# Kernel optimization log

Measured on AMD Instinct MI355X. Metric: run time of the kernel, lower is better.

## Reference

```python
import jax, jax.numpy as jnp
import numpy as np

N, E = 50000, 500000
A, R, EB, EH, H, C, AH, SH, S, AV = 64, 20, 32, 64, 4, 32, 128, 64, 32, 32
EPS = 1e-8
MAX_DIST = 0.5   # nm, maximum_interaction_radius
SCALE = 1.0      # nm, scale_factor


def physnet_rbf(d):
    # PhysNet radial basis: exp(-beta * (exp(-d) - mu_k)^2), mu_k in [exp(-r_cut), 1]
    mu = jnp.linspace(np.exp(-MAX_DIST), 1.0, R).astype(jnp.float32)
    beta = jnp.float32((2.0 / R * (1.0 - np.exp(-MAX_DIST))) ** -2)
    return jnp.exp(-beta * (jnp.exp(-d)[:, None] - mu) ** 2)  # [E, R]


def _forward(h, x, v, idx_i, idx_j, W_edge_in, b_edge_in, W_edge_h, b_edge_h,
             W_edge_out, b_edge_out, W_att, b_att, W_x_mix, W_node1, b_node1,
             W_node2, b_node2, W_post1, b_post1, W_post2, b_post2,
             W_vel1, b_vel1, W_vel2, w_v_mix):
    n = h.shape[0]
    act = jax.nn.silu
    seg_sum = lambda t, idx: jax.ops.segment_sum(t, idx, num_segments=n)

    # geometry
    r_ij = x[idx_j] - x[idx_i]                       # [E,3]
    d_ij = jnp.sqrt(jnp.sum(r_ij * r_ij, -1) + EPS)  # [E]
    dir_ij = r_ij / (d_ij[:, None] + EPS)            # [E,3]

    # update_edge: gather, RBF filter, edge MLP
    h_cat = jnp.concatenate([h[idx_i], h[idx_j]], -1)                 # [E,2A]
    filtered = physnet_rbf(d_ij) * (h_cat @ W_edge_in + b_edge_in)    # [E,R]
    e_in = jnp.concatenate([h_cat, filtered, d_ij[:, None] / SCALE], -1)
    h_ij_edge = act(e_in @ W_edge_h + b_edge_h) @ W_edge_out + b_edge_out  # [E,EB]

    # semantic attention: CELU logits + segment softmax over receivers per head
    logits = jax.nn.celu(h_ij_edge @ W_att + b_att, alpha=2.0)        # [E,H]
    seg_max = jax.ops.segment_max(logits, idx_i, num_segments=n)      # [n,H]
    exp_l = jnp.exp(logits - seg_max[idx_i])
    denom = seg_sum(exp_l, idx_i)
    att = exp_l / (denom[idx_i] + EPS)                                # [E,H]
    h_ij_semantic = (att[:, :, None] * h_ij_edge[:, None, :]).reshape(-1, H * EB)

    # neighborhood aggregation (scatter-add)
    h_i_semantic = seg_sum(h_ij_semantic, idx_i)                      # [n,H*EB]

    # spatial attention
    mix = jnp.tanh(h_ij_semantic @ W_x_mix)                           # [E,C]
    combinations = dir_ij[:, None, :] * mix[:, :, None]               # [E,C,3]
    counts = jnp.maximum(seg_sum(jnp.ones((idx_i.shape[0],), h.dtype), idx_i), 1.0)
    comb_mean = seg_sum(combinations, idx_i) / counts[:, None, None]  # scatter-mean
    comb_norm2 = jnp.sum(comb_mean * comb_mean, -1)                   # [n,C]
    h_i_spatial = act(act(comb_norm2 @ W_post1 + b_post1) @ W_post2 + b_post2)

    # node update (residual)
    node_in = jnp.concatenate([h, h_i_semantic, h_i_spatial], -1)
    h_upd = h + act(act(node_in @ W_node1 + b_node1) @ W_node2 + b_node2)

    # velocity / coordinate update
    v_ij = jnp.einsum('ecx,c->ex', combinations, w_v_mix)             # [E,3]
    dv = seg_sum(v_ij, idx_i) / counts[:, None]                       # scatter-mean
    gate = 2.0 * jax.nn.sigmoid(act(h_upd @ W_vel1 + b_vel1) @ W_vel2)  # [n,1]
    v_upd = gate * v + dv
    x_upd = x + v_upd
    return h_upd, x_upd, v_upd


def _p(k, shape, scale=0.05):
    return jax.random.normal(k, shape, dtype=jnp.float32) * scale


def setup_inputs() -> dict:
    key = jax.random.key(0)
    ks = jax.random.split(key, 24)
    return {
        'h': jax.random.normal(ks[0], (N, A), dtype=jnp.float32),
        'x': jax.random.normal(ks[1], (N, 3), dtype=jnp.float32),
        'v': jax.random.normal(ks[2], (N, 3), dtype=jnp.float32),
        'idx_i': jax.random.randint(ks[3], (E,), 0, N),
        'idx_j': jax.random.randint(ks[4], (E,), 0, N),
        'W_edge_in': _p(ks[5], (2 * A, R)), 'b_edge_in': jnp.zeros((R,), jnp.float32),
        'W_edge_h': _p(ks[6], (2 * A + R + 1, EH)), 'b_edge_h': jnp.zeros((EH,), jnp.float32),
        'W_edge_out': _p(ks[7], (EH, EB)), 'b_edge_out': jnp.zeros((EB,), jnp.float32),
        'W_att': _p(ks[8], (EB, H)), 'b_att': jnp.zeros((H,), jnp.float32),
        'W_x_mix': _p(ks[9], (H * EB, C)),
        'W_node1': _p(ks[10], (A + H * EB + S, AH)), 'b_node1': jnp.zeros((AH,), jnp.float32),
        'W_node2': _p(ks[11], (AH, A)), 'b_node2': jnp.zeros((A,), jnp.float32),
        'W_post1': _p(ks[12], (C, SH)), 'b_post1': jnp.zeros((SH,), jnp.float32),
        'W_post2': _p(ks[13], (SH, S)), 'b_post2': jnp.zeros((S,), jnp.float32),
        'W_vel1': _p(ks[14], (A, AV)), 'b_vel1': jnp.zeros((AV,), jnp.float32),
        'W_vel2': _p(ks[15], (AV, 1)),
        'w_v_mix': _p(ks[16], (C,)),
    }


def reference(h, x, v, idx_i, idx_j, W_edge_in, b_edge_in, W_edge_h, b_edge_h,
              W_edge_out, b_edge_out, W_att, b_att, W_x_mix, W_node1, b_node1,
              W_node2, b_node2, W_post1, b_post1, W_post2, b_post2,
              W_vel1, b_vel1, W_vel2, w_v_mix):
    return _forward(h, x, v, idx_i, idx_j, W_edge_in, b_edge_in, W_edge_h, b_edge_h,
                    W_edge_out, b_edge_out, W_att, b_att, W_x_mix, W_node1, b_node1,
                    W_node2, b_node2, W_post1, b_post1, W_post2, b_post2,
                    W_vel1, b_vel1, W_vel2, w_v_mix)
```

## Files before the change

kernel.cpp:

```cpp
#include <hip/hip_runtime.h>
#include <math.h>

#define DA 64
#define NODEIN_DIM 224
#define EPSC 1e-8f

typedef short v8s __attribute__((ext_vector_type(8)));
typedef float v4f __attribute__((ext_vector_type(4)));
typedef unsigned short ushort_t;

__device__ __forceinline__ float siluf(float v) { return v / (1.0f + __expf(-v)); }

__device__ __forceinline__ void atomAddF(float* p, float v) {
#if defined(__HIP_DEVICE_COMPILE__)
  unsafeAtomicAdd(p, v);
#else
  atomicAdd(p, v);
#endif
}

__device__ __forceinline__ unsigned short f2bfu(float f) {
  union { float f; unsigned u; } v; v.f = f;
  unsigned r = v.u + 0x7fffu + ((v.u >> 16) & 1u);
  return (unsigned short)(r >> 16);
}
__device__ __forceinline__ short f2bfs(float f) { return (short)f2bfu(f); }
__device__ __forceinline__ float bf2f(ushort_t s) {
  union { unsigned u; float f; } v; v.u = ((unsigned)s) << 16; return v.f;
}

#define MU0 0.60653065971263342f
#define DMU ((1.0f - 0.60653065971263342f) / 19.0f)
#define BETA ((float)(1.0 / (0.039346934028736658 * 0.039346934028736658)))

__global__ __launch_bounds__(256) void cast_h(
    const float* __restrict__ hsrc, ushort_t* __restrict__ hb, int n4)
{
  const int i = blockIdx.x * blockDim.x + threadIdx.x;
  if (i < n4) {
    const float4 fv = ((const float4*)hsrc)[i];
    ushort4 o;
    o.x = f2bfu(fv.x); o.y = f2bfu(fv.y); o.z = f2bfu(fv.z); o.w = f2bfu(fv.w);
    ((ushort4*)hb)[i] = o;
  }
}

__global__ __launch_bounds__(256) void deg_count(
    const int* __restrict__ idx_i, int* __restrict__ deg, int E)
{
  const int stride = gridDim.x * blockDim.x;
  for (int e = blockIdx.x * blockDim.x + threadIdx.x; e < E; e += stride)
    atomicAdd(&deg[idx_i[e]], 1);
}

#define SCAN_B 64
#define SCAN_T (SCAN_B * 256)

__global__ __launch_bounds__(256) void deg_tsum(
    const int* __restrict__ deg, int* __restrict__ tsum, int N, int C)
{
  const int g = blockIdx.x * blockDim.x + threadIdx.x;
  const int lo = g * C;
  const int hi = (lo + C < N) ? (lo + C) : N;
  int s = 0;
  for (int i = lo; i < hi; ++i) s += deg[i];
  tsum[g] = s;
}

__global__ __launch_bounds__(256) void scan_tsum(int* __restrict__ tsum)
{
  __shared__ int ps[256];
  const int t = threadIdx.x;
  const int per = SCAN_T / 256;
  const int lo = t * per;
  int s = 0;
  for (int i = 0; i < per; ++i) s += tsum[lo + i];
  ps[t] = s;
  __syncthreads();
  if (t == 0) {
    int a = 0;
    for (int i = 0; i < 256; ++i) { const int v = ps[i]; ps[i] = a; a += v; }
  }
  __syncthreads();
  int acc = ps[t];
  for (int i = 0; i < per; ++i) {
    const int v = tsum[lo + i];
    tsum[lo + i] = acc;
    acc += v;
  }
}

__global__ __launch_bounds__(256) void write_csr(
    const int* __restrict__ deg, const int* __restrict__ tpre,
    int* __restrict__ rowstart, int* __restrict__ cursor,
    float* __restrict__ counts, int N, int C)
{
  const int g = blockIdx.x * blockDim.x + threadIdx.x;
  const int lo = g * C;
  const int hi = (lo + C < N) ? (lo + C) : N;
  int acc = tpre[g];
  for (int i = lo; i < hi; ++i) {
    const int d = deg[i];
    rowstart[i] = acc;
    cursor[i] = acc;
    counts[i] = (float)d;
    acc += d;
  }
  if (hi == N) rowstart[N] = acc;
}

__global__ __launch_bounds__(256) void bucket_edges(
    const int* __restrict__ idx_i, const int* __restrict__ idx_j,
    int* __restrict__ cursor, int* __restrict__ iperm,
    int* __restrict__ jperm, int E)
{
  const int stride = gridDim.x * blockDim.x;
  for (int e = blockIdx.x * blockDim.x + threadIdx.x; e < E; e += stride) {
    const int ii = idx_i[e];
    const int pos = atomicAdd(&cursor[ii], 1);
    iperm[pos] = ii;
    jperm[pos] = idx_j[e];
  }
}

#define THS 72
__global__ __launch_bounds__(256) void edge_f12(
    const ushort_t* __restrict__ h_bf, const float* __restrict__ x,
    const int* __restrict__ iperm, const int* __restrict__ jperm,
    const float* __restrict__ W_in, const float* __restrict__ b_in,
    const float* __restrict__ W_h, const float* __restrict__ b_h,
    const float* __restrict__ W_out, const float* __restrict__ b_out,
    const float* __restrict__ W_att, const float* __restrict__ b_att,
    float* __restrict__ dirb, ushort_t* __restrict__ heb,
    float* __restrict__ expl, float* __restrict__ denom, int E)
{
  __shared__ ushort_t sB1[8 * 512];
  __shared__ ushort_t sB2[20 * 512];
  __shared__ ushort_t tH[4][16 * THS];

  const int tid = threadIdx.x;
  for (int idx = tid; idx < 8 * 512; idx += 256) {
    const int j = idx & 7;
    const int ln = (idx >> 3) & 63;
    const int f = idx >> 9;
    const int k = (f >> 1) * 32 + (ln >> 4) * 8 + j;
    const int col = (f & 1) * 16 + (ln & 15);
    sB1[idx] = (col < 20) ? f2bfu(W_in[k * 20 + col]) : (ushort_t)0;
  }
  for (int idx = tid; idx < 20 * 512; idx += 256) {
    const int j = idx & 7;
    const int ln = (idx >> 3) & 63;
    const int f = idx >> 9;
    const int k = (f >> 2) * 32 + (ln >> 4) * 8 + j;
    const int col = (f & 3) * 16 + (ln & 15);
    sB2[idx] = (k < 149) ? f2bfu(W_h[k * 64 + col]) : (ushort_t)0;
  }
  __syncthreads();

  const int gtid = blockIdx.x * blockDim.x + tid;
  const int wid = gtid >> 6;
  const int lane = tid & 63;
  const int w = tid >> 6;
  const int nw = (gridDim.x * blockDim.x) >> 6;
  const int l15 = lane & 15;
  const int q = lane >> 4;

  const ushort_t* b1l = sB1 + lane * 8;
  const ushort_t* b2l = sB2 + lane * 8;

  v8s bfr3[2][2];
  #pragma unroll
  for (int kc = 0; kc < 2; ++kc)
    #pragma unroll
    for (int nt = 0; nt < 2; ++nt)
      #pragma unroll
      for (int j = 0; j < 8; ++j) {
        const int k = kc * 32 + q * 8 + j;
        const int col = nt * 16 + l15;
        bfr3[kc][nt][j] = f2bfs(W_out[k * 32 + col]);
      }

  float bin[2], mu[2];
  #pragma unroll
  for (int nt = 0; nt < 2; ++nt) {
    const int col = nt * 16 + l15;
    bin[nt] = (col < 20) ? b_in[col] : 0.0f;
    mu[nt] = MU0 + (float)col * DMU;
  }
  float bias2[4];
  #pragma unroll
  for (int nt = 0; nt < 4; ++nt) bias2[nt] = b_h[nt * 16 + l15];
  float bias3[2];
  #pragma unroll
  for (int nt = 0; nt < 2; ++nt) bias3[nt] = b_out[nt * 16 + l15];

  v8s battf;
  #pragma unroll
  for (int j = 0; j < 8; ++j)
    battf[j] = (l15 < 4) ? f2bfs(W_att[(q * 8 + j) * 4 + l15]) : (short)0;
  const float bav = (l15 < 4) ? b_att[l15] : 0.0f;

  const int ntiles = (E + 15) >> 4;

  int iiC = 0, jjC = 0;
  v8s afr[4];
  if (wid < ntiles) {
    const int row0 = wid * 16 + l15;
    const int rowL0 = (row0 < E) ? row0 : (E - 1);
    iiC = iperm[rowL0];
    jjC = jperm[rowL0];
    afr[0] = *(const v8s*)(h_bf + (size_t)iiC * 64 + q * 8);
    afr[1] = *(const v8s*)(h_bf + (size_t)iiC * 64 + 32 + q * 8);
    afr[2] = *(const v8s*)(h_bf + (size_t)jjC * 64 + q * 8);
    afr[3] = *(const v8s*)(h_bf + (size_t)jjC * 64 + 32 + q * 8);
  }

  for (int t = wid; t < ntiles; t += nw) {
    const int tn = t + nw;
    int iiN = 0, jjN = 0;
    v8s nfr[4];
    if (tn < ntiles) {
      const int rowN = tn * 16 + l15;
      const int rowLN = (rowN < E) ? rowN : (E - 1);
      iiN = iperm[rowLN];
      jjN = jperm[rowLN];
      nfr[0] = *(const v8s*)(h_bf + (size_t)iiN * 64 + q * 8);
      nfr[1] = *(const v8s*)(h_bf + (size_t)iiN * 64 + 32 + q * 8);
      nfr[2] = *(const v8s*)(h_bf + (size_t)jjN * 64 + q * 8);
      nfr[3] = *(const v8s*)(h_bf + (size_t)jjN * 64 + 32 + q * 8);
    }

    const int row = t * 16 + l15;
    float dval = 0.0f;
    if (lane < 16 && row < E) {
      const float rx = x[jjC * 3 + 0] - x[iiC * 3 + 0];
      const float ry = x[jjC * 3 + 1] - x[iiC * 3 + 1];
      const float rz = x[jjC * 3 + 2] - x[iiC * 3 + 2];
      const float d = sqrtf(rx * rx + ry * ry + rz * rz + EPSC);
      dval = d;
      const float inv = 1.0f / (d + EPSC);
      dirb[row * 3 + 0] = rx * inv;
      dirb[row * 3 + 1] = ry * inv;
      dirb[row * 3 + 2] = rz * inv;
    }

    v4f acc1[2];
    #pragma unroll
    for (int nt = 0; nt < 2; ++nt) {
      v4f a = {0.f, 0.f, 0.f, 0.f};
      #pragma unroll
      for (int kc = 0; kc < 4; ++kc) {
        const v8s bfrag = *(const v8s*)(b1l + (kc * 2 + nt) * 512);
        a = __builtin_amdgcn_mfma_f32_16x16x32_bf16(afr[kc], bfrag, a, 0, 0, 0);
      }
      acc1[nt] = a;
    }

    float dr[4], edr[4];
    #pragma unroll
    for (int r = 0; r < 4; ++r) {
      dr[r] = __shfl(dval, q * 4 + r);
      edr[r] = __expf(-dr[r]);
    }
    #pragma unroll
    for (int nt = 0; nt < 2; ++nt) {
      const int col = nt * 16 + l15;
      #pragma unroll
      for (int r = 0; r < 4; ++r) {
        ushort_t ov;
        if (col < 20) {
          const float tt = edr[r] - mu[nt];
          ov = f2bfu((acc1[nt][r] + bin[nt]) * __expf(-BETA * tt * tt));
        } else if (col == 20) {
          ov = f2bfu(dr[r]);
        } else {
          ov = 0;
        }
        tH[w][(q * 4 + r) * THS + col] = ov;
      }
    }
    __builtin_amdgcn_wave_barrier();

    const v8s afr4 = *(const v8s*)&tH[w][l15 * THS + q * 8];
    __builtin_amdgcn_wave_barrier();

    v4f acc2[4];
    #pragma unroll
    for (int nt = 0; nt < 4; ++nt) {
      v4f a = {0.f, 0.f, 0.f, 0.f};
      #pragma unroll
      for (int kc = 0; kc < 4; ++kc) {
        const v8s bfrag = *(const v8s*)(b2l + (kc * 4 + nt) * 512);
        a = __builtin_amdgcn_mfma_f32_16x16x32_bf16(afr[kc], bfrag, a, 0, 0, 0);
      }
      const v8s bfrag4 = *(const v8s*)(b2l + (4 * 4 + nt) * 512);
      a = __builtin_amdgcn_mfma_f32_16x16x32_bf16(afr4, bfrag4, a, 0, 0, 0);
      acc2[nt] = a;
    }

    #pragma unroll
    for (int nt = 0; nt < 4; ++nt) {
      #pragma unroll
      for (int r = 0; r < 4; ++r)
        tH[w][(q * 4 + r) * THS + nt * 16 + l15] =
            f2bfu(siluf(acc2[nt][r] + bias2[nt]));
    }
    __builtin_amdgcn_wave_barrier();

    v8s af3[2];
    af3[0] = *(const v8s*)&tH[w][l15 * THS + q * 8];
    af3[1] = *(const v8s*)&tH[w][l15 * THS + 32 + q * 8];

    v4f acc3[2];
    #pragma unroll
    for (int nt = 0; nt < 2; ++nt) {
      v4f a = {0.f, 0.f, 0.f, 0.f};
      #pragma unroll
      for (int kc = 0; kc < 2; ++kc)
        a = __builtin_amdgcn_mfma_f32_16x16x32_bf16(af3[kc], bfr3[kc][nt], a, 0, 0, 0);
      acc3[nt] = a;
    }
    __builtin_amdgcn_wave_barrier();

    const int rowb = t * 16 + q * 4;
    #pragma unroll
    for (int nt = 0; nt < 2; ++nt) {
      const int col = nt * 16 + l15;
      #pragma unroll
      for (int r = 0; r < 4; ++r) {
        const ushort_t hv = f2bfu(acc3[nt][r] + bias3[nt]);
        tH[w][(q * 4 + r) * THS + col] = hv;
        if (rowb + r < E) heb[(size_t)(rowb + r) * 32 + col] = hv;
      }
    }
    __builtin_amdgcn_wave_barrier();

    const v8s afA = *(const v8s*)&tH[w][l15 * THS + q * 8];
    v4f az = {0.f, 0.f, 0.f, 0.f};
    const v4f aacc = __builtin_amdgcn_mfma_f32_16x16x32_bf16(afA, battf, az, 0, 0, 0);

    int ii_r[4];
    #pragma unroll
    for (int r = 0; r < 4; ++r) ii_r[r] = __shfl(iiC, q * 4 + r);

    if (l15 < 4) {
      #pragma unroll
      for (int r = 0; r < 4; ++r) {
        if (rowb + r < E) {
          const float la = aacc[r] + bav;
          const float l = (la > 0.f) ? la : 2.0f * (__expf(0.5f * la) - 1.0f);
          const float ev = __expf(l);
          expl[(size_t)(rowb + r) * 4 + l15] = ev;
          atomAddF(&denom[ii_r[r] * 4 + l15], ev);
        }
      }
    }
    __builtin_amdgcn_wave_barrier();

    iiC = iiN; jjC = jjN;
    afr[0] = nfr[0]; afr[1] = nfr[1]; afr[2] = nfr[2]; afr[3] = nfr[3];
  }
}

__global__ __launch_bounds__(256) void mix_kernel(
    const ushort_t* __restrict__ heb, const int* __restrict__ iperm,
    const float* __restrict__ expl, const float* __restrict__ denom,
    const float* __restrict__ W_xmix, const float* __restrict__ w_vmix,
    ushort_t* __restrict__ mixE, float* __restrict__ pE, int E)
{
  const int tid = blockIdx.x * blockDim.x + threadIdx.x;
  const int wid = tid >> 6;
  const int lane = threadIdx.x & 63;
  const int nw = (gridDim.x * blockDim.x) >> 6;
  const int l15 = lane & 15;
  const int q = lane >> 4;

  v8s bfr[4][2];
  #pragma unroll
  for (int kc = 0; kc < 4; ++kc)
    #pragma unroll
    for (int nt = 0; nt < 2; ++nt)
      #pragma unroll
      for (int j = 0; j < 8; ++j) {
        const int k = kc * 32 + q * 8 + j;
        const int col = nt * 16 + l15;
        bfr[kc][nt][j] = f2bfs(W_xmix[k * 32 + col]);
      }
  float wv[2];
  wv[0] = w_vmix[l15];
  wv[1] = w_vmix[16 + l15];

  const int ntiles = (E + 15) >> 4;
  for (int t = wid; t < ntiles; t += nw) {
    const int row = t * 16 + l15;
    const int rowL = (row < E) ? row : (E - 1);
    const int ii = iperm[rowL];
    float att[4];
    #pragma unroll
    for (int hh = 0; hh < 4; ++hh)
      att[hh] = expl[(size_t)rowL * 4 + hh] / (denom[ii * 4 + hh] + EPSC);

    const v8s hech = *(const v8s*)(heb + (size_t)rowL * 32 + q * 8);
    float hef[8];
    #pragma unroll
    for (int j = 0; j < 8; ++j) hef[j] = bf2f((ushort_t)hech[j]);

    v8s afr[4];
    #pragma unroll
    for (int kc = 0; kc < 4; ++kc)
      #pragma unroll
      for (int j = 0; j < 8; ++j)
        afr[kc][j] = f2bfs(att[kc] * hef[j]);

    v4f acc[2];
    #pragma unroll
    for (int nt = 0; nt < 2; ++nt) {
      v4f a = {0.f, 0.f, 0.f, 0.f};
      #pragma unroll
      for (int kc = 0; kc < 4; ++kc)
        a = __builtin_amdgcn_mfma_f32_16x16x32_bf16(afr[kc], bfr[kc][nt], a, 0, 0, 0);
      acc[nt] = a;
    }

    const int rowb = t * 16 + q * 4;
    float pr[4];
    #pragma unroll
    for (int r = 0; r < 4; ++r) {
      const float m0 = tanhf(acc[0][r]);
      const float m1 = tanhf(acc[1][r]);
      if (rowb + r < E) {
        mixE[(size_t)(rowb + r) * 32 + l15] = f2bfu(m0);
        mixE[(size_t)(rowb + r) * 32 + 16 + l15] = f2bfu(m1);
      }
      pr[r] = m0 * wv[0] + m1 * wv[1];
    }
    #pragma unroll
    for (int r = 0; r < 4; ++r) {
      pr[r] += __shfl_xor(pr[r], 1);
      pr[r] += __shfl_xor(pr[r], 2);
      pr[r] += __shfl_xor(pr[r], 4);
      pr[r] += __shfl_xor(pr[r], 8);
      if (l15 == 0 && rowb + r < E) pE[rowb + r] = pr[r];
    }
  }
}

__global__ __launch_bounds__(256) void node_reduce(
    const int* __restrict__ rowstart,
    const ushort_t* __restrict__ heb, const ushort_t* __restrict__ mixE,
    const float* __restrict__ expl, const float* __restrict__ denom,
    const float* __restrict__ dirb, const float* __restrict__ pE,
    ushort_t* __restrict__ hsem, float* __restrict__ comb_sum,
    float* __restrict__ dv_sum, int N)
{
  const int tid = blockIdx.x * blockDim.x + threadIdx.x;
  const int wid = tid >> 6;
  const int lane = threadIdx.x & 63;
  const int nw = (gridDim.x * blockDim.x) >> 6;
  const int hh = lane >> 5;
  const int eb = lane & 31;

  for (int n = wid; n < N; n += nw) {
    const int s = rowstart[n];
    const int epd = rowstart[n + 1];
    float semA = 0.f, semB = 0.f;
    float cx = 0.f, cy = 0.f, cz = 0.f;
    float dvx = 0.f, dvy = 0.f, dvz = 0.f;
    int k = s;
    const int e4 = s + ((epd - s) & ~3);
    for (; k < e4; k += 4) {
      float he[4], ea[4], ec[4], dx[4], dy[4], dz[4], m[4], pe[4];
      #pragma unroll
      for (int u = 0; u < 4; ++u) {
        he[u] = bf2f(heb[(size_t)(k + u) * 32 + eb]);
        ea[u] = expl[(size_t)(k + u) * 4 + hh];
        ec[u] = expl[(size_t)(k + u) * 4 + 2 + hh];
        dx[u] = dirb[(k + u) * 3 + 0];
        dy[u] = dirb[(k + u) * 3 + 1];
        dz[u] = dirb[(k + u) * 3 + 2];
      }
      if (lane < 32) {
        #pragma unroll
        for (int u = 0; u < 4; ++u)
          m[u] = bf2f(mixE[(size_t)(k + u) * 32 + lane]);
      }
      if (lane == 0) {
        #pragma unroll
        for (int u = 0; u < 4; ++u) pe[u] = pE[k + u];
      }
      #pragma unroll
      for (int u = 0; u < 4; ++u) {
        semA += ea[u] * he[u];
        semB += ec[u] * he[u];
        if (lane < 32) {
          cx += dx[u] * m[u]; cy += dy[u] * m[u]; cz += dz[u] * m[u];
        }
        if (lane == 0) {
          dvx += dx[u] * pe[u]; dvy += dy[u] * pe[u]; dvz += dz[u] * pe[u];
        }
      }
    }
    for (; k < epd; ++k) {
      const float he = bf2f(heb[(size_t)k * 32 + eb]);
      const float ea = expl[(size_t)k * 4 + hh];
      const float ec = expl[(size_t)k * 4 + 2 + hh];
      semA += ea * he;
      semB += ec * he;
      const float dx = dirb[k * 3 + 0];
      const float dy = dirb[k * 3 + 1];
      const float dz = dirb[k * 3 + 2];
      if (lane < 32) {
        const float m = bf2f(mixE[(size_t)k * 32 + lane]);
        cx += dx * m; cy += dy * m; cz += dz * m;
      }
      if (lane == 0) {
        const float pe = pE[k];
        dvx += dx * pe; dvy += dy * pe; dvz += dz * pe;
      }
    }
    const float dA = denom[n * 4 + hh] + EPSC;
    const float dB = denom[n * 4 + 2 + hh] + EPSC;
    hsem[(size_t)n * 128 + lane] = f2bfu(semA / dA);
    hsem[(size_t)n * 128 + 64 + lane] = f2bfu(semB / dB);
    if (lane < 32) {
      comb_sum[(size_t)n * 96 + lane * 3 + 0] = cx;
      comb_sum[(size_t)n * 96 + lane * 3 + 1] = cy;
      comb_sum[(size_t)n * 96 + lane * 3 + 2] = cz;
    }
    if (lane == 0) {
      dv_sum[n * 3 + 0] = dvx;
      dv_sum[n * 3 + 1] = dvy;
      dv_sum[n * 3 + 2] = dvz;
    }
  }
}

#define W1S 232
__global__ __launch_bounds__(256) void node_c1_mfma(
    const ushort_t* __restrict__ h_bf, const ushort_t* __restrict__ hsem,
    const float* __restrict__ comb_sum, const float* __restrict__ counts,
    const float* __restrict__ W_post1, const float* __restrict__ b_post1,
    const float* __restrict__ W_post2, const float* __restrict__ b_post2,
    const float* __restrict__ W_node1, const float* __restrict__ b_node1,
    ushort_t* __restrict__ nh_out, int N)
{
  __shared__ ushort_t sW1t[128 * W1S];
  __shared__ ushort_t tp[4][16 * THS];

  const int tid = threadIdx.x;
  for (int idx = tid; idx < 224 * 128; idx += 256) {
    const int k = idx >> 7;
    const int c = idx & 127;
    sW1t[c * W1S + k] = f2bfu(W_node1[idx]);
  }
  __syncthreads();

  const int lane = tid & 63;
  const int w = tid >> 6;
  const int l15 = lane & 15;
  const int q = lane >> 4;

  v8s bp1[4];
  #pragma unroll
  for (int nt = 0; nt < 4; ++nt)
    #pragma unroll
    for (int j = 0; j < 8; ++j)
      bp1[nt][j] = f2bfs(W_post1[(q * 8 + j) * 64 + nt * 16 + l15]);
  v8s bp2[2][2];
  #pragma unroll
  for (int kc = 0; kc < 2; ++kc)
    #pragma unroll
    for (int nt = 0; nt < 2; ++nt)
      #pragma unroll
      for (int j = 0; j < 8; ++j)
        bp2[kc][nt][j] = f2bfs(W_post2[(kc * 32 + q * 8 + j) * 32 + nt * 16 + l15]);
  float bb1[4];
  #pragma unroll
  for (int nt = 0; nt < 4; ++nt) bb1[nt] = b_post1[nt * 16 + l15];
  float bb2[2];
  #pragma unroll
  for (int nt = 0; nt < 2; ++nt) bb2[nt] = b_post2[nt * 16 + l15];
  float b1[8];
  #pragma unroll
  for (int nt = 0; nt < 8; ++nt) b1[nt] = b_node1[nt * 16 + l15];

  const int gw = blockIdx.x * 4 + w;
  const int nwv = gridDim.x * 4;
  const int ntiles = (N + 15) >> 4;

  for (int t = gw; t < ntiles; t += nwv) {
    const int row = t * 16 + l15;
    const int rowL = (row < N) ? row : (N - 1);

    const float inv = 1.0f / fmaxf(counts[rowL], 1.0f);
    const float4* cs = (const float4*)(comb_sum + (size_t)rowL * 96 + q * 24);
    float cf[24];
    #pragma unroll
    for (int b = 0; b < 6; ++b) {
      const float4 cv = cs[b];
      cf[b * 4 + 0] = cv.x; cf[b * 4 + 1] = cv.y;
      cf[b * 4 + 2] = cv.z; cf[b * 4 + 3] = cv.w;
    }
    v8s a1;
    #pragma unroll
    for (int j = 0; j < 8; ++j) {
      const float vx = cf[j * 3 + 0] * inv;
      const float vy = cf[j * 3 + 1] * inv;
      const float vz = cf[j * 3 + 2] * inv;
      a1[j] = f2bfs(vx * vx + vy * vy + vz * vz);
    }

    v4f p1[4];
    #pragma unroll
    for (int nt = 0; nt < 4; ++nt) {
      v4f a = {0.f, 0.f, 0.f, 0.f};
      p1[nt] = __builtin_amdgcn_mfma_f32_16x16x32_bf16(a1, bp1[nt], a, 0, 0, 0);
    }
    #pragma unroll
    for (int nt = 0; nt < 4; ++nt)
      #pragma unroll
      for (int r = 0; r < 4; ++r)
        tp[w][(q * 4 + r) * THS + nt * 16 + l15] =
            f2bfu(siluf(p1[nt][r] + bb1[nt]));
    __builtin_amdgcn_wave_barrier();

    v8s a2[2];
    a2[0] = *(const v8s*)&tp[w][l15 * THS + q * 8];
    a2[1] = *(const v8s*)&tp[w][l15 * THS + 32 + q * 8];

    v4f p2[2];
    #pragma unroll
    for (int nt = 0; nt < 2; ++nt) {
      v4f a = {0.f, 0.f, 0.f, 0.f};
      #pragma unroll
      for (int kc = 0; kc < 2; ++kc)
        a = __builtin_amdgcn_mfma_f32_16x16x32_bf16(a2[kc], bp2[kc][nt], a, 0, 0, 0);
      p2[nt] = a;
    }
    __builtin_amdgcn_wave_barrier();
    #pragma unroll
    for (int nt = 0; nt < 2; ++nt)
      #pragma unroll
      for (int r = 0; r < 4; ++r)
        tp[w][(q * 4 + r) * THS + nt * 16 + l15] =
            f2bfu(siluf(p2[nt][r] + bb2[nt]));
    __builtin_amdgcn_wave_barrier();

    v8s af[7];
    af[0] = *(const v8s*)(h_bf + (size_t)rowL * 64 + q * 8);
    af[1] = *(const v8s*)(h_bf + (size_t)rowL * 64 + 32 + q * 8);
    #pragma unroll
    for (int kc = 0; kc < 4; ++kc)
      af[2 + kc] = *(const v8s*)(hsem + (size_t)rowL * 128 + kc * 32 + q * 8);
    af[6] = *(const v8s*)&tp[w][l15 * THS + q * 8];

    v4f acc[8];
    #pragma unroll
    for (int nt = 0; nt < 8; ++nt) acc[nt] = (v4f){0.f, 0.f, 0.f, 0.f};
    #pragma unroll
    for (int kc = 0; kc < 7; ++kc) {
      #pragma unroll
      for (int nt = 0; nt < 8; ++nt) {
        const v8s bfrag =
            *(const v8s*)&sW1t[(nt * 16 + l15) * W1S + kc * 32 + q * 8];
        acc[nt] = __builtin_amdgcn_mfma_f32_16x16x32_bf16(af[kc], bfrag, acc[nt], 0, 0, 0);
      }
    }

    const int rowb = t * 16 + q * 4;
    #pragma unroll
    for (int nt = 0; nt < 8; ++nt) {
      #pragma unroll
      for (int r = 0; r < 4; ++r)
        if (rowb + r < N)
          nh_out[(size_t)(rowb + r) * 128 + nt * 16 + l15] =
              f2bfu(siluf(acc[nt][r] + b1[nt]));
    }
  }
}

__global__ __launch_bounds__(256) void node_c2_mfma(
    const float* __restrict__ h, const float* __restrict__ x,
    const float* __restrict__ v, const ushort_t* __restrict__ nh,
    const float* __restrict__ dv_sum, const float* __restrict__ counts,
    const float* __restrict__ W_node2, const float* __restrict__ b_node2,
    const float* __restrict__ W_vel1, const float* __restrict__ b_vel1,
    const float* __restrict__ W_vel2,
    float* __restrict__ out, int N)
{
  __shared__ ushort_t sW2[16 * 64 * 8];
  __shared__ ushort_t sWv[4 * 64 * 8];
  __shared__ ushort_t tH[4][16 * THS];
  __shared__ float sg[4][16];

  const int tid = threadIdx.x;
  for (int idx = tid; idx < 16 * 64 * 8; idx += 256) {
    const int j = idx & 7;
    const int ln = (idx >> 3) & 63;
    const int f = idx >> 9;
    const int k = (f >> 2) * 32 + (ln >> 4) * 8 + j;
    const int col = (f & 3) * 16 + (ln & 15);
    sW2[idx] = f2bfu(W_node2[k * 64 + col]);
  }
  for (int idx = tid; idx < 4 * 64 * 8; idx += 256) {
    const int j = idx & 7;
    const int ln = (idx >> 3) & 63;
    const int f = idx >> 9;
    const int k = (f >> 1) * 32 + (ln >> 4) * 8 + j;
    const int col = (f & 1) * 16 + (ln & 15);
    sWv[idx] = f2bfu(W_vel1[k * 32 + col]);
  }
  __syncthreads();

  const int lane = tid & 63;
  const int w = tid >> 6;
  const int l15 = lane & 15;
  const int q = lane >> 4;

  const ushort_t* w2l = sW2 + lane * 8;
  const ushort_t* wvl = sWv + lane * 8;

  float b2[4];
  #pragma unroll
  for (int nt = 0; nt < 4; ++nt) b2[nt] = b_node2[nt * 16 + l15];
  float bv[2];
  #pragma unroll
  for (int nt = 0; nt < 2; ++nt) bv[nt] = b_vel1[nt * 16 + l15];
  float wv2[2];
  #pragma unroll
  for (int nt = 0; nt < 2; ++nt) wv2[nt] = W_vel2[nt * 16 + l15];

  const int gw = blockIdx.x * 4 + w;
  const int nwv = gridDim.x * 4;
  const int ntiles = (N + 15) >> 4;

  for (int t = gw; t < ntiles; t += nwv) {
    const int row = t * 16 + l15;
    const int rowL = (row < N) ? row : (N - 1);

    v8s af[4];
    #pragma unroll
    for (int kc = 0; kc < 4; ++kc)
      af[kc] = *(const v8s*)(nh + (size_t)rowL * 128 + kc * 32 + q * 8);

    v4f acc[4];
    #pragma unroll
    for (int nt = 0; nt < 4; ++nt) {
      v4f a = {0.f, 0.f, 0.f, 0.f};
      #pragma unroll
      for (int kc = 0; kc < 4; ++kc) {
        const v8s bfrag = *(const v8s*)(w2l + (kc * 4 + nt) * 512);
        a = __builtin_amdgcn_mfma_f32_16x16x32_bf16(af[kc], bfrag, a, 0, 0, 0);
      }
      acc[nt] = a;
    }

    const int rowb = t * 16 + q * 4;
    #pragma unroll
    for (int nt = 0; nt < 4; ++nt) {
      const int col = nt * 16 + l15;
      #pragma unroll
      for (int r = 0; r < 4; ++r) {
        const int n = rowb + r;
        if (n < N) {
          const float hu = h[(size_t)n * 64 + col] + siluf(acc[nt][r] + b2[nt]);
          out[(size_t)n * 64 + col] = hu;
          tH[w][(q * 4 + r) * THS + col] = f2bfu(hu);
        }
      }
    }
    __builtin_amdgcn_wave_barrier();

    v8s a2[2];
    a2[0] = *(const v8s*)&tH[w][l15 * THS + q * 8];
    a2[1] = *(const v8s*)&tH[w][l15 * THS + 32 + q * 8];
    v4f av[2];
    #pragma unroll
    for (int nt = 0; nt < 2; ++nt) {
      v4f a = {0.f, 0.f, 0.f, 0.f};
      #pragma unroll
      for (int kc = 0; kc < 2; ++kc) {
        const v8s bfrag = *(const v8s*)(wvl + (kc * 2 + nt) * 512);
        a = __builtin_amdgcn_mfma_f32_16x16x32_bf16(a2[kc], bfrag, a, 0, 0, 0);
      }
      av[nt] = a;
    }

    #pragma unroll
    for (int r = 0; r < 4; ++r) {
      float pr = siluf(av[0][r] + bv[0]) * wv2[0] +
                 siluf(av[1][r] + bv[1]) * wv2[1];
      pr += __shfl_xor(pr, 1);
      pr += __shfl_xor(pr, 2);
      pr += __shfl_xor(pr, 4);
      pr += __shfl_xor(pr, 8);
      if (l15 == 0) sg[w][q * 4 + r] = 2.0f / (1.0f + __expf(-pr));
    }
    __builtin_amdgcn_wave_barrier();

    if (lane < 48) {
      const int rr = lane / 3;
      const int c = lane % 3;
      const int n = t * 16 + rr;
      if (n < N) {
        const float gate = sg[w][rr];
        const float cnt = fmaxf(counts[n], 1.0f);
        const float dv = dv_sum[n * 3 + c] / cnt;
        const float vu = gate * v[n * 3 + c] + dv;
        out[(size_t)N * 64 + (size_t)n * 3 + c] = x[n * 3 + c] + vu;
        out[(size_t)N * 64 + (size_t)N * 3 + (size_t)n * 3 + c] = vu;
      }
    }
    __builtin_amdgcn_wave_barrier();
  }
}

extern "C" void kernel_launch(void* const* d_in, const int* in_sizes, int n_in,
                              void* d_out, int out_size, void* d_ws, size_t ws_size,
                              hipStream_t stream) {
  const float* h   = (const float*)d_in[0];
  const float* x   = (const float*)d_in[1];
  const float* v   = (const float*)d_in[2];
  const int* idx_i = (const int*)d_in[3];
  const int* idx_j = (const int*)d_in[4];
  const float* W_edge_in  = (const float*)d_in[5];
  const float* b_edge_in  = (const float*)d_in[6];
  const float* W_edge_h   = (const float*)d_in[7];
  const float* b_edge_h   = (const float*)d_in[8];
  const float* W_edge_out = (const float*)d_in[9];
  const float* b_edge_out = (const float*)d_in[10];
  const float* W_att      = (const float*)d_in[11];
  const float* b_att      = (const float*)d_in[12];
  const float* W_x_mix    = (const float*)d_in[13];
  const float* W_node1    = (const float*)d_in[14];
  const float* b_node1    = (const float*)d_in[15];
  const float* W_node2    = (const float*)d_in[16];
  const float* b_node2    = (const float*)d_in[17];
  const float* W_post1    = (const float*)d_in[18];
  const float* b_post1    = (const float*)d_in[19];
  const float* W_post2    = (const float*)d_in[20];
  const float* b_post2    = (const float*)d_in[21];
  const float* W_vel1     = (const float*)d_in[22];
  const float* b_vel1     = (const float*)d_in[23];
  const float* W_vel2     = (const float*)d_in[24];
  const float* w_v_mix    = (const float*)d_in[25];

  const int E = in_sizes[3];
  const int N = in_sizes[0] / DA;

  float* ws = (float*)d_ws;
  size_t off = 0;
  float* denom    = ws + off; off += (size_t)N * 4;
  int*   deg      = (int*)(ws + off); off += (size_t)N;
  const size_t zeroBytes = off * sizeof(float);
  float* counts   = ws + off; off += (size_t)N;
  int*   rowstart = (int*)(ws + off); off += (size_t)N + 4;
  int*   cursor   = (int*)(ws + off); off += (size_t)N;
  int*   tsum     = (int*)(ws + off); off += (size_t)SCAN_T;
  int*   iperm    = (int*)(ws + off); off += (size_t)E;
  int*   jperm    = (int*)(ws + off); off += (size_t)E;
  float* pE       = ws + off; off += (size_t)E;
  float* expl     = ws + off; off += (size_t)E * 4;
  float* dirb     = ws + off; off += (size_t)E * 3;
  float* hsemR    = ws + off; off += (size_t)N * 64;
  float* comb_sum = ws + off; off += (size_t)N * 96;
  float* dv_sum   = ws + off; off += (size_t)N * 4;
  float* hbfR     = ws + off; off += (size_t)N * 32;
  float* fltR     = ws + off; off += (size_t)E * 16;
  float* hebR     = ws + off; off += (size_t)E * 16;

  ushort_t* h_bf = (ushort_t*)hbfR;
  ushort_t* hsem = (ushort_t*)hsemR;
  ushort_t* heb  = (ushort_t*)hebR;
  ushort_t* mixE = (ushort_t*)fltR;
  ushort_t* nh   = (ushort_t*)fltR;

  hipMemsetAsync(d_ws, 0, zeroBytes, stream);

  {
    const int n4 = (N * 64) / 4;
    cast_h<<<(n4 + 255) / 256, 256, 0, stream>>>(h, h_bf, n4);
  }
  deg_count<<<512, 256, 0, stream>>>(idx_i, deg, E);
  {
    const int C = (N + SCAN_T - 1) / SCAN_T;
    deg_tsum<<<SCAN_B, 256, 0, stream>>>(deg, tsum, N, C);
    scan_tsum<<<1, 256, 0, stream>>>(tsum);
    write_csr<<<SCAN_B, 256, 0, stream>>>(deg, tsum, rowstart, cursor, counts, N, C);
  }
  bucket_edges<<<512, 256, 0, stream>>>(idx_i, idx_j, cursor, iperm, jperm, E);
  edge_f12<<<1024, 256, 0, stream>>>(h_bf, x, iperm, jperm,
                                     W_edge_in, b_edge_in, W_edge_h, b_edge_h,
                                     W_edge_out, b_edge_out, W_att, b_att,
                                     dirb, heb, expl, denom, E);
  mix_kernel<<<1024, 256, 0, stream>>>(heb, iperm, expl, denom, W_x_mix,
                                       w_v_mix, mixE, pE, E);
  node_reduce<<<2048, 256, 0, stream>>>(rowstart, heb, mixE, expl, denom,
                                        dirb, pE, hsem, comb_sum, dv_sum, N);
  node_c1_mfma<<<512, 256, 0, stream>>>(
      h_bf, hsem, comb_sum, counts, W_post1, b_post1, W_post2, b_post2,
      W_node1, b_node1, nh, N);
  node_c2_mfma<<<512, 256, 0, stream>>>(
      h, x, v, nh, dv_sum, counts, W_node2, b_node2, W_vel1, b_vel1, W_vel2,
      (float*)d_out, N);
}
```

Before: 417.4 us.

## Fuse mix projection into node reduction and precompute mean norms

```diff
diff --git a/kernel.cpp b/kernel.cpp
--- a/kernel.cpp
+++ b/kernel.cpp
@@ -9,7 +9,12 @@
 typedef float v4f __attribute__((ext_vector_type(4)));
 typedef unsigned short ushort_t;
 
-__device__ __forceinline__ float siluf(float v) { return v / (1.0f + __expf(-v)); }
+__device__ __forceinline__ float siluf(float v) {
+  return v * __builtin_amdgcn_rcpf(1.0f + __expf(-v));
+}
+__device__ __forceinline__ float tanhfast(float x) {
+  return 1.0f - 2.0f * __builtin_amdgcn_rcpf(__expf(2.0f * x) + 1.0f);
+}
 
 __device__ __forceinline__ void atomAddF(float* p, float v) {
 #if defined(__HIP_DEVICE_COMPILE__)
@@ -92,8 +97,7 @@
 
 __global__ __launch_bounds__(256) void write_csr(
     const int* __restrict__ deg, const int* __restrict__ tpre,
-    int* __restrict__ rowstart, int* __restrict__ cursor,
-    float* __restrict__ counts, int N, int C)
+    int* __restrict__ rowstart, int* __restrict__ cursor, int N, int C)
 {
   const int g = blockIdx.x * blockDim.x + threadIdx.x;
   const int lo = g * C;
@@ -103,7 +107,6 @@
     const int d = deg[i];
     rowstart[i] = acc;
     cursor[i] = acc;
-    counts[i] = (float)d;
     acc += d;
   }
   if (hi == N) rowstart[N] = acc;
@@ -204,6 +207,7 @@
 
   int iiC = 0, jjC = 0;
   v8s afr[4];
+  float rCx = 0.f, rCy = 0.f, rCz = 0.f;
   if (wid < ntiles) {
     const int row0 = wid * 16 + l15;
     const int rowL0 = (row0 < E) ? row0 : (E - 1);
@@ -213,12 +217,18 @@
     afr[1] = *(const v8s*)(h_bf + (size_t)iiC * 64 + 32 + q * 8);
     afr[2] = *(const v8s*)(h_bf + (size_t)jjC * 64 + q * 8);
     afr[3] = *(const v8s*)(h_bf + (size_t)jjC * 64 + 32 + q * 8);
+    if (lane < 16) {
+      rCx = x[jjC * 3 + 0] - x[iiC * 3 + 0];
+      rCy = x[jjC * 3 + 1] - x[iiC * 3 + 1];
+      rCz = x[jjC * 3 + 2] - x[iiC * 3 + 2];
+    }
   }
 
   for (int t = wid; t < ntiles; t += nw) {
     const int tn = t + nw;
     int iiN = 0, jjN = 0;
     v8s nfr[4];
+    float rNx = 0.f, rNy = 0.f, rNz = 0.f;
     if (tn < ntiles) {
       const int rowN = tn * 16 + l15;
       const int rowLN = (rowN < E) ? rowN : (E - 1);
@@ -228,20 +238,24 @@
       nfr[1] = *(const v8s*)(h_bf + (size_t)iiN * 64 + 32 + q * 8);
       nfr[2] = *(const v8s*)(h_bf + (size_t)jjN * 64 + q * 8);
       nfr[3] = *(const v8s*)(h_bf + (size_t)jjN * 64 + 32 + q * 8);
+      if (lane < 16) {
+        rNx = x[jjN * 3 + 0] - x[iiN * 3 + 0];
+        rNy = x[jjN * 3 + 1] - x[iiN * 3 + 1];
+        rNz = x[jjN * 3 + 2] - x[iiN * 3 + 2];
+      }
     }
 
     const int row = t * 16 + l15;
     float dval = 0.0f;
-    if (lane < 16 && row < E) {
-      const float rx = x[jjC * 3 + 0] - x[iiC * 3 + 0];
-      const float ry = x[jjC * 3 + 1] - x[iiC * 3 + 1];
-      const float rz = x[jjC * 3 + 2] - x[iiC * 3 + 2];
-      const float d = sqrtf(rx * rx + ry * ry + rz * rz + EPSC);
-      dval = d;
-      const float inv = 1.0f / (d + EPSC);
-      dirb[row * 3 + 0] = rx * inv;
-      dirb[row * 3 + 1] = ry * inv;
-      dirb[row * 3 + 2] = rz * inv;
+    if (lane < 16) {
+      const float s2 = rCx * rCx + rCy * rCy + rCz * rCz + EPSC;
+      const float rv = __builtin_amdgcn_rsqf(s2);
+      dval = s2 * rv;
+      if (row < E) {
+        dirb[row * 3 + 0] = rCx * rv;
+        dirb[row * 3 + 1] = rCy * rv;
+        dirb[row * 3 + 2] = rCz * rv;
+      }
     }
 
     v4f acc1[2];
@@ -359,178 +373,148 @@
 
     iiC = iiN; jjC = jjN;
     afr[0] = nfr[0]; afr[1] = nfr[1]; afr[2] = nfr[2]; afr[3] = nfr[3];
-  }
-}
-
-__global__ __launch_bounds__(256) void mix_kernel(
-    const ushort_t* __restrict__ heb, const int* __restrict__ iperm,
+    rCx = rNx; rCy = rNy; rCz = rNz;
+  }
+}
+
+__global__ __launch_bounds__(256) void node_fused(
+    const int* __restrict__ rowstart,
+    const ushort_t* __restrict__ heb,
     const float* __restrict__ expl, const float* __restrict__ denom,
+    const float* __restrict__ dirb,
     const float* __restrict__ W_xmix, const float* __restrict__ w_vmix,
-    ushort_t* __restrict__ mixE, float* __restrict__ pE, int E)
-{
-  const int tid = blockIdx.x * blockDim.x + threadIdx.x;
-  const int wid = tid >> 6;
-  const int lane = threadIdx.x & 63;
+    ushort_t* __restrict__ hsem, float* __restrict__ norm2,
+    float* __restrict__ dv_mean, int N)
+{
+  __shared__ ushort_t sBX[8 * 512];
+
+  const int tid = threadIdx.x;
+  for (int idx = tid; idx < 8 * 512; idx += 256) {
+    const int j = idx & 7;
+    const int ln = (idx >> 3) & 63;
+    const int f = idx >> 9;
+    const int k = (f >> 1) * 32 + (ln >> 4) * 8 + j;
+    const int col = (f & 1) * 16 + (ln & 15);
+    sBX[idx] = f2bfu(W_xmix[k * 32 + col]);
+  }
+  __syncthreads();
+
+  const int gtid = blockIdx.x * blockDim.x + tid;
+  const int wid = gtid >> 6;
+  const int lane = tid & 63;
   const int nw = (gridDim.x * blockDim.x) >> 6;
   const int l15 = lane & 15;
   const int q = lane >> 4;
-
-  v8s bfr[4][2];
-  #pragma unroll
-  for (int kc = 0; kc < 4; ++kc)
-    #pragma unroll
-    for (int nt = 0; nt < 2; ++nt)
-      #pragma unroll
-      for (int j = 0; j < 8; ++j) {
-        const int k = kc * 32 + q * 8 + j;
-        const int col = nt * 16 + l15;
-        bfr[kc][nt][j] = f2bfs(W_xmix[k * 32 + col]);
-      }
-  float wv[2];
-  wv[0] = w_vmix[l15];
-  wv[1] = w_vmix[16 + l15];
-
-  const int ntiles = (E + 15) >> 4;
-  for (int t = wid; t < ntiles; t += nw) {
-    const int row = t * 16 + l15;
-    const int rowL = (row < E) ? row : (E - 1);
-    const int ii = iperm[rowL];
-    float att[4];
-    #pragma unroll
-    for (int hh = 0; hh < 4; ++hh)
-      att[hh] = expl[(size_t)rowL * 4 + hh] / (denom[ii * 4 + hh] + EPSC);
-
-    const v8s hech = *(const v8s*)(heb + (size_t)rowL * 32 + q * 8);
-    float hef[8];
-    #pragma unroll
-    for (int j = 0; j < 8; ++j) hef[j] = bf2f((ushort_t)hech[j]);
-
-    v8s afr[4];
-    #pragma unroll
-    for (int kc = 0; kc < 4; ++kc)
-      #pragma unroll
-      for (int j = 0; j < 8; ++j)
-        afr[kc][j] = f2bfs(att[kc] * hef[j]);
-
-    v4f acc[2];
-    #pragma unroll
-    for (int nt = 0; nt < 2; ++nt) {
-      v4f a = {0.f, 0.f, 0.f, 0.f};
-      #pragma unroll
-      for (int kc = 0; kc < 4; ++kc)
-        a = __builtin_amdgcn_mfma_f32_16x16x32_bf16(afr[kc], bfr[kc][nt], a, 0, 0, 0);
-      acc[nt] = a;
-    }
-
-    const int rowb = t * 16 + q * 4;
-    float pr[4];
-    #pragma unroll
-    for (int r = 0; r < 4; ++r) {
-      const float m0 = tanhf(acc[0][r]);
-      const float m1 = tanhf(acc[1][r]);
-      if (rowb + r < E) {
-        mixE[(size_t)(rowb + r) * 32 + l15] = f2bfu(m0);
-        mixE[(size_t)(rowb + r) * 32 + 16 + l15] = f2bfu(m1);
-      }
-      pr[r] = m0 * wv[0] + m1 * wv[1];
-    }
-    #pragma unroll
-    for (int r = 0; r < 4; ++r) {
-      pr[r] += __shfl_xor(pr[r], 1);
-      pr[r] += __shfl_xor(pr[r], 2);
-      pr[r] += __shfl_xor(pr[r], 4);
-      pr[r] += __shfl_xor(pr[r], 8);
-      if (l15 == 0 && rowb + r < E) pE[rowb + r] = pr[r];
-    }
-  }
-}
-
-__global__ __launch_bounds__(256) void node_reduce(
-    const int* __restrict__ rowstart,
-    const ushort_t* __restrict__ heb, const ushort_t* __restrict__ mixE,
-    const float* __restrict__ expl, const float* __restrict__ denom,
-    const float* __restrict__ dirb, const float* __restrict__ pE,
-    ushort_t* __restrict__ hsem, float* __restrict__ comb_sum,
-    float* __restrict__ dv_sum, int N)
-{
-  const int tid = blockIdx.x * blockDim.x + threadIdx.x;
-  const int wid = tid >> 6;
-  const int lane = threadIdx.x & 63;
-  const int nw = (gridDim.x * blockDim.x) >> 6;
   const int hh = lane >> 5;
   const int eb = lane & 31;
+  const ushort_t* bXl = sBX + lane * 8;
+
+  const float wv0 = w_vmix[l15];
+  const float wv1 = w_vmix[16 + l15];
 
   for (int n = wid; n < N; n += nw) {
     const int s = rowstart[n];
     const int epd = rowstart[n + 1];
+    const int deg = epd - s;
+
+    float invden[4];
+    #pragma unroll
+    for (int h4 = 0; h4 < 4; ++h4)
+      invden[h4] = __builtin_amdgcn_rcpf(denom[n * 4 + h4] + EPSC);
+
     float semA = 0.f, semB = 0.f;
-    float cx = 0.f, cy = 0.f, cz = 0.f;
+    {
+      int k = s;
+      const int e4 = s + (deg & ~3);
+      for (; k < e4; k += 4) {
+        #pragma unroll
+        for (int u = 0; u < 4; ++u) {
+          const float he = bf2f(heb[(size_t)(k + u) * 32 + eb]);
+          semA += expl[(size_t)(k + u) * 4 + hh] * he;
+          semB += expl[(size_t)(k + u) * 4 + 2 + hh] * he;
+        }
+      }
+      for (; k < epd; ++k) {
+        const float he = bf2f(heb[(size_t)k * 32 + eb]);
+        semA += expl[(size_t)k * 4 + hh] * he;
+        semB += expl[(size_t)k * 4 + 2 + hh] * he;
+      }
+    }
+    hsem[(size_t)n * 128 + lane] = f2bfu(semA * invden[hh]);
+    hsem[(size_t)n * 128 + 64 + lane] = f2bfu(semB * invden[2 + hh]);
+
+    float cx0 = 0.f, cy0 = 0.f, cz0 = 0.f;
+    float cx1 = 0.f, cy1 = 0.f, cz1 = 0.f;
     float dvx = 0.f, dvy = 0.f, dvz = 0.f;
-    int k = s;
-    const int e4 = s + ((epd - s) & ~3);
-    for (; k < e4; k += 4) {
-      float he[4], ea[4], ec[4], dx[4], dy[4], dz[4], m[4], pe[4];
-      #pragma unroll
-      for (int u = 0; u < 4; ++u) {
-        he[u] = bf2f(heb[(size_t)(k + u) * 32 + eb]);
-        ea[u] = expl[(size_t)(k + u) * 4 + hh];
-        ec[u] = expl[(size_t)(k + u) * 4 + 2 + hh];
-        dx[u] = dirb[(k + u) * 3 + 0];
-        dy[u] = dirb[(k + u) * 3 + 1];
-        dz[u] = dirb[(k + u) * 3 + 2];
-      }
-      if (lane < 32) {
+
+    for (int c0 = 0; c0 < deg; c0 += 16) {
+      const int ra = c0 + l15;
+      const int eA = s + ((ra < deg) ? ra : (deg - 1));
+      const v8s hech = *(const v8s*)(heb + (size_t)eA * 32 + q * 8);
+
+      v4f y[4][2];
+      #pragma unroll
+      for (int h4 = 0; h4 < 4; ++h4) {
         #pragma unroll
-        for (int u = 0; u < 4; ++u)
-          m[u] = bf2f(mixE[(size_t)(k + u) * 32 + lane]);
-      }
-      if (lane == 0) {
-        #pragma unroll
-        for (int u = 0; u < 4; ++u) pe[u] = pE[k + u];
-      }
-      #pragma unroll
-      for (int u = 0; u < 4; ++u) {
-        semA += ea[u] * he[u];
-        semB += ec[u] * he[u];
-        if (lane < 32) {
-          cx += dx[u] * m[u]; cy += dy[u] * m[u]; cz += dz[u] * m[u];
+        for (int nt = 0; nt < 2; ++nt) {
+          v4f z = {0.f, 0.f, 0.f, 0.f};
+          y[h4][nt] = __builtin_amdgcn_mfma_f32_16x16x32_bf16(
+              hech, *(const v8s*)(bXl + (h4 * 2 + nt) * 512), z, 0, 0, 0);
         }
-        if (lane == 0) {
-          dvx += dx[u] * pe[u]; dvy += dy[u] * pe[u]; dvz += dz[u] * pe[u];
-        }
-      }
-    }
-    for (; k < epd; ++k) {
-      const float he = bf2f(heb[(size_t)k * 32 + eb]);
-      const float ea = expl[(size_t)k * 4 + hh];
-      const float ec = expl[(size_t)k * 4 + 2 + hh];
-      semA += ea * he;
-      semB += ec * he;
-      const float dx = dirb[k * 3 + 0];
-      const float dy = dirb[k * 3 + 1];
-      const float dz = dirb[k * 3 + 2];
-      if (lane < 32) {
-        const float m = bf2f(mixE[(size_t)k * 32 + lane]);
-        cx += dx * m; cy += dy * m; cz += dz * m;
-      }
-      if (lane == 0) {
-        const float pe = pE[k];
-        dvx += dx * pe; dvy += dy * pe; dvz += dz * pe;
-      }
-    }
-    const float dA = denom[n * 4 + hh] + EPSC;
-    const float dB = denom[n * 4 + 2 + hh] + EPSC;
-    hsem[(size_t)n * 128 + lane] = f2bfu(semA / dA);
-    hsem[(size_t)n * 128 + 64 + lane] = f2bfu(semB / dB);
-    if (lane < 32) {
-      comb_sum[(size_t)n * 96 + lane * 3 + 0] = cx;
-      comb_sum[(size_t)n * 96 + lane * 3 + 1] = cy;
-      comb_sum[(size_t)n * 96 + lane * 3 + 2] = cz;
+      }
+
+      #pragma unroll
+      for (int r = 0; r < 4; ++r) {
+        const int rr = c0 + q * 4 + r;
+        const int live = rr < deg;
+        const int eR = s + (live ? rr : (deg - 1));
+        const float lf = live ? 1.0f : 0.0f;
+        const float4 ex4 = *(const float4*)(expl + (size_t)eR * 4);
+        const float at0 = ex4.x * invden[0] * lf;
+        const float at1 = ex4.y * invden[1] * lf;
+        const float at2 = ex4.z * invden[2] * lf;
+        const float at3 = ex4.w * invden[3] * lf;
+        const float p0 = at0 * y[0][0][r] + at1 * y[1][0][r] +
+                         at2 * y[2][0][r] + at3 * y[3][0][r];
+        const float p1 = at0 * y[0][1][r] + at1 * y[1][1][r] +
+                         at2 * y[2][1][r] + at3 * y[3][1][r];
+        const float dx = dirb[eR * 3 + 0];
+        const float dy = dirb[eR * 3 + 1];
+        const float dz = dirb[eR * 3 + 2];
+        const float m0 = tanhfast(p0);
+        const float m1 = tanhfast(p1);
+        cx0 += dx * m0; cy0 += dy * m0; cz0 += dz * m0;
+        cx1 += dx * m1; cy1 += dy * m1; cz1 += dz * m1;
+        float pr = m0 * wv0 + m1 * wv1;
+        pr += __shfl_xor(pr, 1);
+        pr += __shfl_xor(pr, 2);
+        pr += __shfl_xor(pr, 4);
+        pr += __shfl_xor(pr, 8);
+        if (l15 == 0) { dvx += pr * dx; dvy += pr * dy; dvz += pr * dz; }
+      }
+    }
+
+    cx0 += __shfl_xor(cx0, 16); cx0 += __shfl_xor(cx0, 32);
+    cy0 += __shfl_xor(cy0, 16); cy0 += __shfl_xor(cy0, 32);
+    cz0 += __shfl_xor(cz0, 16); cz0 += __shfl_xor(cz0, 32);
+    cx1 += __shfl_xor(cx1, 16); cx1 += __shfl_xor(cx1, 32);
+    cy1 += __shfl_xor(cy1, 16); cy1 += __shfl_xor(cy1, 32);
+    cz1 += __shfl_xor(cz1, 16); cz1 += __shfl_xor(cz1, 32);
+    dvx += __shfl_xor(dvx, 16); dvx += __shfl_xor(dvx, 32);
+    dvy += __shfl_xor(dvy, 16); dvy += __shfl_xor(dvy, 32);
+    dvz += __shfl_xor(dvz, 16); dvz += __shfl_xor(dvz, 32);
+
+    const float cinv = __builtin_amdgcn_rcpf(fmaxf((float)deg, 1.0f));
+    if (lane < 16) {
+      const float mx0 = cx0 * cinv, my0 = cy0 * cinv, mz0 = cz0 * cinv;
+      norm2[(size_t)n * 32 + l15] = mx0 * mx0 + my0 * my0 + mz0 * mz0;
+      const float mx1 = cx1 * cinv, my1 = cy1 * cinv, mz1 = cz1 * cinv;
+      norm2[(size_t)n * 32 + 16 + l15] = mx1 * mx1 + my1 * my1 + mz1 * mz1;
     }
     if (lane == 0) {
-      dv_sum[n * 3 + 0] = dvx;
-      dv_sum[n * 3 + 1] = dvy;
-      dv_sum[n * 3 + 2] = dvz;
+      dv_mean[n * 3 + 0] = dvx * cinv;
+      dv_mean[n * 3 + 1] = dvy * cinv;
+      dv_mean[n * 3 + 2] = dvz * cinv;
     }
   }
 }
@@ -538,7 +522,7 @@
 #define W1S 232
 __global__ __launch_bounds__(256) void node_c1_mfma(
     const ushort_t* __restrict__ h_bf, const ushort_t* __restrict__ hsem,
-    const float* __restrict__ comb_sum, const float* __restrict__ counts,
+    const float* __restrict__ norm2,
     const float* __restrict__ W_post1, const float* __restrict__ b_post1,
     const float* __restrict__ W_post2, const float* __restrict__ b_post2,
     const float* __restrict__ W_node1, const float* __restrict__ b_node1,
@@ -592,23 +576,13 @@
     const int row = t * 16 + l15;
     const int rowL = (row < N) ? row : (N - 1);
 
-    const float inv = 1.0f / fmaxf(counts[rowL], 1.0f);
-    const float4* cs = (const float4*)(comb_sum + (size_t)rowL * 96 + q * 24);
-    float cf[24];
-    #pragma unroll
-    for (int b = 0; b < 6; ++b) {
-      const float4 cv = cs[b];
-      cf[b * 4 + 0] = cv.x; cf[b * 4 + 1] = cv.y;
-      cf[b * 4 + 2] = cv.z; cf[b * 4 + 3] = cv.w;
-    }
+    const float4 nA = *(const float4*)(norm2 + (size_t)rowL * 32 + q * 8);
+    const float4 nB = *(const float4*)(norm2 + (size_t)rowL * 32 + q * 8 + 4);
     v8s a1;
-    #pragma unroll
-    for (int j = 0; j < 8; ++j) {
-      const float vx = cf[j * 3 + 0] * inv;
-      const float vy = cf[j * 3 + 1] * inv;
-      const float vz = cf[j * 3 + 2] * inv;
-      a1[j] = f2bfs(vx * vx + vy * vy + vz * vz);
-    }
+    a1[0] = f2bfs(nA.x); a1[1] = f2bfs(nA.y);
+    a1[2] = f2bfs(nA.z); a1[3] = f2bfs(nA.w);
+    a1[4] = f2bfs(nB.x); a1[5] = f2bfs(nB.y);
+    a1[6] = f2bfs(nB.z); a1[7] = f2bfs(nB.w);
 
     v4f p1[4];
     #pragma unroll
@@ -682,7 +656,7 @@
 __global__ __launch_bounds__(256) void node_c2_mfma(
     const float* __restrict__ h, const float* __restrict__ x,
     const float* __restrict__ v, const ushort_t* __restrict__ nh,
-    const float* __restrict__ dv_sum, const float* __restrict__ counts,
+    const float* __restrict__ dv_mean,
     const float* __restrict__ W_node2, const float* __restrict__ b_node2,
     const float* __restrict__ W_vel1, const float* __restrict__ b_vel1,
     const float* __restrict__ W_vel2,
@@ -794,7 +768,8 @@
       pr += __shfl_xor(pr, 2);
       pr += __shfl_xor(pr, 4);
       pr += __shfl_xor(pr, 8);
-      if (l15 == 0) sg[w][q * 4 + r] = 2.0f / (1.0f + __expf(-pr));
+      if (l15 == 0)
+        sg[w][q * 4 + r] = 2.0f * __builtin_amdgcn_rcpf(1.0f + __expf(-pr));
     }
     __builtin_amdgcn_wave_barrier();
 
@@ -804,8 +779,7 @@
       const int n = t * 16 + rr;
       if (n < N) {
         const float gate = sg[w][rr];
-        const float cnt = fmaxf(counts[n], 1.0f);
-        const float dv = dv_sum[n * 3 + c] / cnt;
+        const float dv = dv_mean[n * 3 + c];
         const float vu = gate * v[n * 3 + c] + dv;
         out[(size_t)N * 64 + (size_t)n * 3 + c] = x[n * 3 + c] + vu;
         out[(size_t)N * 64 + (size_t)N * 3 + (size_t)n * 3 + c] = vu;
@@ -853,18 +827,16 @@
   float* denom    = ws + off; off += (size_t)N * 4;
   int*   deg      = (int*)(ws + off); off += (size_t)N;
   const size_t zeroBytes = off * sizeof(float);
-  float* counts   = ws + off; off += (size_t)N;
   int*   rowstart = (int*)(ws + off); off += (size_t)N + 4;
   int*   cursor   = (int*)(ws + off); off += (size_t)N;
   int*   tsum     = (int*)(ws + off); off += (size_t)SCAN_T;
   int*   iperm    = (int*)(ws + off); off += (size_t)E;
   int*   jperm    = (int*)(ws + off); off += (size_t)E;
-  float* pE       = ws + off; off += (size_t)E;
   float* expl     = ws + off; off += (size_t)E * 4;
   float* dirb     = ws + off; off += (size_t)E * 3;
   float* hsemR    = ws + off; off += (size_t)N * 64;
-  float* comb_sum = ws + off; off += (size_t)N * 96;
-  float* dv_sum   = ws + off; off += (size_t)N * 4;
+  float* norm2    = ws + off; off += (size_t)N * 32;
+  float* dv_mean  = ws + off; off += (size_t)N * 4;
   float* hbfR     = ws + off; off += (size_t)N * 32;
   float* fltR     = ws + off; off += (size_t)E * 16;
   float* hebR     = ws + off; off += (size_t)E * 16;
@@ -872,7 +844,6 @@
   ushort_t* h_bf = (ushort_t*)hbfR;
   ushort_t* hsem = (ushort_t*)hsemR;
   ushort_t* heb  = (ushort_t*)hebR;
-  ushort_t* mixE = (ushort_t*)fltR;
   ushort_t* nh   = (ushort_t*)fltR;
 
   hipMemsetAsync(d_ws, 0, zeroBytes, stream);
@@ -886,21 +857,20 @@
     const int C = (N + SCAN_T - 1) / SCAN_T;
     deg_tsum<<<SCAN_B, 256, 0, stream>>>(deg, tsum, N, C);
     scan_tsum<<<1, 256, 0, stream>>>(tsum);
-    write_csr<<<SCAN_B, 256, 0, stream>>>(deg, tsum, rowstart, cursor, counts, N, C);
+    write_csr<<<SCAN_B, 256, 0, stream>>>(deg, tsum, rowstart, cursor, N, C);
   }
   bucket_edges<<<512, 256, 0, stream>>>(idx_i, idx_j, cursor, iperm, jperm, E);
   edge_f12<<<1024, 256, 0, stream>>>(h_bf, x, iperm, jperm,
                                      W_edge_in, b_edge_in, W_edge_h, b_edge_h,
                                      W_edge_out, b_edge_out, W_att, b_att,
                                      dirb, heb, expl, denom, E);
-  mix_kernel<<<1024, 256, 0, stream>>>(heb, iperm, expl, denom, W_x_mix,
-                                       w_v_mix, mixE, pE, E);
-  node_reduce<<<2048, 256, 0, stream>>>(rowstart, heb, mixE, expl, denom,
-                                        dirb, pE, hsem, comb_sum, dv_sum, N);
+  node_fused<<<2048, 256, 0, stream>>>(rowstart, heb, expl, denom, dirb,
+                                       W_x_mix, w_v_mix, hsem, norm2,
+                                       dv_mean, N);
   node_c1_mfma<<<512, 256, 0, stream>>>(
-      h_bf, hsem, comb_sum, counts, W_post1, b_post1, W_post2, b_post2,
+      h_bf, hsem, norm2, W_post1, b_post1, W_post2, b_post2,
       W_node1, b_node1, nh, N);
   node_c2_mfma<<<512, 256, 0, stream>>>(
-      h, x, v, nh, dv_sum, counts, W_node2, b_node2, W_vel1, b_vel1, W_vel2,
+      h, x, v, nh, dv_mean, W_node2, b_node2, W_vel1, b_vel1, W_vel2,
       (float*)d_out, N);
 }
```

After: 387.5 us. 1.08x faster.
